# Optimization experiments

Measured on AMD Instinct MI355X. Metric: run time of the kernel, lower is better.

## Reference

```python
import jax, jax.numpy as jnp
import numpy as np

IM_H = 256.0
IM_W = 256.0


def setup_inputs() -> dict:
    key = jax.random.key(0)
    k1, k2 = jax.random.split(key)
    feats = jax.random.normal(k1, (8, 64, 64, 64), dtype=jnp.float32)
    Kcam = jax.random.normal(k2, (2, 4, 3, 4), dtype=jnp.float32)
    vmax = jnp.ones((2, 3), dtype=jnp.float32)
    vmin = jnp.zeros((2, 3), dtype=jnp.float32)
    return {"feats": feats, "Kcam": Kcam, "vmax": vmax, "vmin": vmin, "nvox": 48}


def reference(feats, Kcam, vmax, vmin, nvox):
    nR, fdim, fh, fw = feats.shape
    batch, view = Kcam.shape[0], Kcam.shape[1]
    rsz_h = float(fh) / IM_H
    rsz_w = float(fw) / IM_W

    # Build voxel grid per batch: linspace(vmin, vmax, nvox) along each axis.
    t = jnp.linspace(0.0, 1.0, nvox, dtype=jnp.float32)  # [nvox]
    rng = vmin[:, :, None] + (vmax - vmin)[:, :, None] * t  # [batch, 3, nvox]
    shp = (batch, nvox, nvox, nvox)
    gx = jnp.broadcast_to(rng[:, 0, :, None, None], shp)  # meshgrid 'ij' (torch default)
    gy = jnp.broadcast_to(rng[:, 1, None, :, None], shp)
    gz = jnp.broadcast_to(rng[:, 2, None, None, :], shp)
    grid = jnp.stack([gx, gy, gz], axis=1).reshape(batch, 3, -1)  # [batch, 3, nV]
    nV = grid.shape[2]
    rs_grid = jnp.concatenate([grid, jnp.ones((batch, 1, nV), jnp.float32)], axis=1)  # [batch, 4, nV]

    # Perspective projection: [batch, view*3, 4] @ [batch, 4, nV]
    im_p = jnp.einsum('bvrk,bkn->bvrn', Kcam, rs_grid).reshape(batch * view, 3, nV)
    im_x, im_y, im_z = im_p[:, 0, :], im_p[:, 1, :], im_p[:, 2, :]
    im_x = jnp.clip(im_x / im_z * rsz_w, 0.0, fw - 1)
    im_y = jnp.clip(im_y / im_z * rsz_h, 0.0, fh - 1)

    im_x0 = jnp.floor(im_x)
    im_x1 = jnp.clip(im_x0 + 1.0, 0.0, fw - 1)
    im_y0 = jnp.floor(im_y)
    im_y1 = jnp.clip(im_y0 + 1.0, 0.0, fh - 1)

    flat = feats.reshape(nR, fdim, fh * fw)  # [nR, fdim, fh*fw]

    def gather(xi, yi):
        idx = (yi * fw + xi).astype(jnp.int32)  # [nR, nV]
        return jax.vmap(lambda f, i: f[:, i])(flat, idx)  # [nR, fdim, nV]

    Ia = gather(im_x0, im_y0)
    Ib = gather(im_x0, im_y1)
    Ic = gather(im_x1, im_y0)
    Id = gather(im_x1, im_y1)

    wa = ((im_x1 - im_x) * (im_y1 - im_y))[:, None, :]
    wb = ((im_x1 - im_x) * (im_y - im_y0))[:, None, :]
    wc = ((im_x - im_x0) * (im_y1 - im_y))[:, None, :]
    wd = ((im_x - im_x0) * (im_y - im_y0))[:, None, :]

    Ibilin = wa * Ia + wb * Ib + wc * Ic + wd * Id  # [nR, fdim, nV]
    return Ibilin.reshape(nR, fdim, nvox, nvox, nvox)
```

## Files before the change

kernel.cpp:

```cpp
#include <hip/hip_runtime.h>


#define NR    8
#define FDIM  64
#define FH    64
#define FW    64
#define NVOX  48
#define NV    (NVOX * NVOX * NVOX)
#define VIEW  4

__global__ __launch_bounds__(256) void proj_splat_kernel(
    const float* __restrict__ feats,
    const float* __restrict__ Kcam,
    const float* __restrict__ vmax,
    const float* __restrict__ vmin,
    float* __restrict__ out)
{
    const int r = blockIdx.y;
    const int n = blockIdx.x * 256 + threadIdx.x;
    const int b = r >> 2;

    const int i   = n / (NVOX * NVOX);
    const int rem = n - i * (NVOX * NVOX);
    const int j   = rem / NVOX;
    const int k   = rem - j * NVOX;

    const float inv = 1.0f / (float)(NVOX - 1);
    const float tx = (float)i * inv;
    const float ty = (float)j * inv;
    const float tz = (float)k * inv;

    const float* vmn = vmin + b * 3;
    const float* vmx = vmax + b * 3;
    const float gx = vmn[0] + (vmx[0] - vmn[0]) * tx;
    const float gy = vmn[1] + (vmx[1] - vmn[1]) * ty;
    const float gz = vmn[2] + (vmx[2] - vmn[2]) * tz;

    const float* K = Kcam + r * 12;
    const float px = K[0] * gx + K[1] * gy + K[2]  * gz + K[3];
    const float py = K[4] * gx + K[5] * gy + K[6]  * gz + K[7];
    const float pz = K[8] * gx + K[9] * gy + K[10] * gz + K[11];

    const float rsz_w = (float)FW / 256.0f;
    const float rsz_h = (float)FH / 256.0f;

    float imx = px / pz * rsz_w;
    float imy = py / pz * rsz_h;
    imx = fminf(fmaxf(imx, 0.0f), (float)(FW - 1));
    imy = fminf(fmaxf(imy, 0.0f), (float)(FH - 1));

    const float x0 = floorf(imx);
    const float x1 = fminf(x0 + 1.0f, (float)(FW - 1));
    const float y0 = floorf(imy);
    const float y1 = fminf(y0 + 1.0f, (float)(FH - 1));

    const float wa = (x1 - imx) * (y1 - imy);
    const float wb = (x1 - imx) * (imy - y0);
    const float wc = (imx - x0) * (y1 - imy);
    const float wd = (imx - x0) * (imy - y0);

    const int ix0 = (int)x0, ix1 = (int)x1;
    const int iy0 = (int)y0, iy1 = (int)y1;
    const int i00 = iy0 * FW + ix0;
    const int i10 = iy1 * FW + ix0;
    const int i01 = iy0 * FW + ix1;
    const int i11 = iy1 * FW + ix1;

    const float* f = feats + (size_t)r * FDIM * FH * FW;
    float* o = out + (size_t)r * FDIM * NV + n;

#pragma unroll 4
    for (int c = 0; c < FDIM; ++c) {
        const float* fc = f + c * (FH * FW);
        const float Ia = fc[i00];
        const float Ib = fc[i10];
        const float Ic = fc[i01];
        const float Id = fc[i11];
        const float v = wa * Ia + wb * Ib + wc * Ic + wd * Id;
        __builtin_nontemporal_store(v, o + (size_t)c * NV);
    }
}

extern "C" void kernel_launch(void* const* d_in, const int* in_sizes, int n_in,
                              void* d_out, int out_size, void* d_ws, size_t ws_size,
                              hipStream_t stream) {
    const float* feats = (const float*)d_in[0];
    const float* Kcam  = (const float*)d_in[1];
    const float* vmax  = (const float*)d_in[2];
    const float* vmin  = (const float*)d_in[3];
    float* out = (float*)d_out;

    dim3 grid(NV / 256, NR);
    dim3 block(256);
    proj_splat_kernel<<<grid, block, 0, stream>>>(feats, Kcam, vmax, vmin, out);
}
```

Baseline: 274.9 us.

## Stage feature channels in LDS and compute four voxels per thread

Each block now takes a 16x8x16 voxel tile for one view. It streams the feature image through shared memory two channels at a time, prefetching the next pair into registers while the current pair is used. Each thread projects four consecutive z-voxels once, reads the bilinear taps from LDS instead of scattered global loads, and writes float4 nontemporal stores. This replaces per-voxel random global gathers with coalesced image loads and LDS lookups. In exchange, every tile re-reads the whole feature volume for its view, syncs twice per channel pair, and the grid shrinks to 432 blocks of 512 threads, which may leave some CUs idle.

```diff
diff --git a/kernel.cpp b/kernel.cpp
--- a/kernel.cpp
+++ b/kernel.cpp
@@ -5,79 +5,134 @@
 #define FDIM  64
 #define FH    64
 #define FW    64
+#define IMG   (FH * FW)
 #define NVOX  48
 #define NV    (NVOX * NVOX * NVOX)
-#define VIEW  4
+#define CPP   2
+#define NPH   (FDIM / CPP)
+#define TI    16
+#define TJ    8
+#define TK    16
+#define THREADS 512
 
-__global__ __launch_bounds__(256) void proj_splat_kernel(
+typedef float f32x4 __attribute__((ext_vector_type(4)));
+
+__global__ __launch_bounds__(THREADS, 4) void proj_splat_kernel(
     const float* __restrict__ feats,
     const float* __restrict__ Kcam,
     const float* __restrict__ vmax,
     const float* __restrict__ vmin,
     float* __restrict__ out)
 {
+    __shared__ float lds[CPP][IMG + 4];
+
+    const int t = threadIdx.x;
     const int r = blockIdx.y;
-    const int n = blockIdx.x * 256 + threadIdx.x;
     const int b = r >> 2;
 
-    const int i   = n / (NVOX * NVOX);
-    const int rem = n - i * (NVOX * NVOX);
-    const int j   = rem / NVOX;
-    const int k   = rem - j * NVOX;
+    const int tile = blockIdx.x;
+    const int ti = tile / 18;
+    const int tj = (tile / 3) % 6;
+    const int tk = tile % 3;
+
+    const int i_loc = t >> 5;
+    const int j_loc = (t >> 2) & 7;
+    const int k4    = t & 3;
+
+    const int vi  = ti * TI + i_loc;
+    const int vj  = tj * TJ + j_loc;
+    const int vk0 = tk * TK + k4 * 4;
 
     const float inv = 1.0f / (float)(NVOX - 1);
-    const float tx = (float)i * inv;
-    const float ty = (float)j * inv;
-    const float tz = (float)k * inv;
-
     const float* vmn = vmin + b * 3;
     const float* vmx = vmax + b * 3;
-    const float gx = vmn[0] + (vmx[0] - vmn[0]) * tx;
-    const float gy = vmn[1] + (vmx[1] - vmn[1]) * ty;
-    const float gz = vmn[2] + (vmx[2] - vmn[2]) * tz;
+    const float gx = vmn[0] + (vmx[0] - vmn[0]) * ((float)vi * inv);
+    const float gy = vmn[1] + (vmx[1] - vmn[1]) * ((float)vj * inv);
 
     const float* K = Kcam + r * 12;
-    const float px = K[0] * gx + K[1] * gy + K[2]  * gz + K[3];
-    const float py = K[4] * gx + K[5] * gy + K[6]  * gz + K[7];
-    const float pz = K[8] * gx + K[9] * gy + K[10] * gz + K[11];
+    const float pxc = K[0] * gx + K[1] * gy + K[3];
+    const float pyc = K[4] * gx + K[5] * gy + K[7];
+    const float pzc = K[8] * gx + K[9] * gy + K[11];
 
-    const float rsz_w = (float)FW / 256.0f;
-    const float rsz_h = (float)FH / 256.0f;
+    const float rsz = 0.25f;
 
-    float imx = px / pz * rsz_w;
-    float imy = py / pz * rsz_h;
-    imx = fminf(fmaxf(imx, 0.0f), (float)(FW - 1));
-    imy = fminf(fmaxf(imy, 0.0f), (float)(FH - 1));
+    int   idxA[4], idxB[4];
+    float wA0[4], wA1[4], wB0[4], wB1[4];
+#pragma unroll
+    for (int v = 0; v < 4; ++v) {
+        const float gz = vmn[2] + (vmx[2] - vmn[2]) * ((float)(vk0 + v) * inv);
+        const float px = pxc + K[2]  * gz;
+        const float py = pyc + K[6]  * gz;
+        const float pz = pzc + K[10] * gz;
 
-    const float x0 = floorf(imx);
-    const float x1 = fminf(x0 + 1.0f, (float)(FW - 1));
-    const float y0 = floorf(imy);
-    const float y1 = fminf(y0 + 1.0f, (float)(FH - 1));
+        float imx = px / pz * rsz;
+        float imy = py / pz * rsz;
+        imx = fminf(fmaxf(imx, 0.0f), (float)(FW - 1));
+        imy = fminf(fmaxf(imy, 0.0f), (float)(FH - 1));
 
-    const float wa = (x1 - imx) * (y1 - imy);
-    const float wb = (x1 - imx) * (imy - y0);
-    const float wc = (imx - x0) * (y1 - imy);
-    const float wd = (imx - x0) * (imy - y0);
+        const float x0 = floorf(imx);
+        const float x1 = fminf(x0 + 1.0f, (float)(FW - 1));
+        const float y0 = floorf(imy);
+        const float y1 = fminf(y0 + 1.0f, (float)(FH - 1));
 
-    const int ix0 = (int)x0, ix1 = (int)x1;
-    const int iy0 = (int)y0, iy1 = (int)y1;
-    const int i00 = iy0 * FW + ix0;
-    const int i10 = iy1 * FW + ix0;
-    const int i01 = iy0 * FW + ix1;
-    const int i11 = iy1 * FW + ix1;
+        wA0[v] = (x1 - imx) * (y1 - imy);
+        wA1[v] = (imx - x0) * (y1 - imy);
+        wB0[v] = (x1 - imx) * (imy - y0);
+        wB1[v] = (imx - x0) * (imy - y0);
 
-    const float* f = feats + (size_t)r * FDIM * FH * FW;
-    float* o = out + (size_t)r * FDIM * NV + n;
+        const int ix0 = (int)x0;
+        const int iy0 = (int)y0;
+        const int iy1 = (int)y1;
+        idxA[v] = iy0 * FW + ix0;
+        idxB[v] = iy1 * FW + ix0;
+    }
 
-#pragma unroll 4
-    for (int c = 0; c < FDIM; ++c) {
-        const float* fc = f + c * (FH * FW);
-        const float Ia = fc[i00];
-        const float Ib = fc[i10];
-        const float Ic = fc[i01];
-        const float Id = fc[i11];
-        const float v = wa * Ia + wb * Ib + wc * Ic + wd * Id;
-        __builtin_nontemporal_store(v, o + (size_t)c * NV);
+    if (t == 0) { lds[0][IMG] = 0.0f; lds[1][IMG] = 0.0f; }
+
+    const float* fbase = feats + (size_t)r * FDIM * IMG;
+    float* obase = out + (size_t)r * FDIM * NV + ((vi * NVOX + vj) * NVOX + vk0);
+
+    f32x4 sreg[2][CPP];
+#pragma unroll
+    for (int ci = 0; ci < CPP; ++ci)
+#pragma unroll
+        for (int q = 0; q < 2; ++q)
+            sreg[q][ci] = *reinterpret_cast<const f32x4*>(
+                fbase + (size_t)ci * IMG + q * 2048 + t * 4);
+
+    for (int p = 0; p < NPH; ++p) {
+#pragma unroll
+        for (int ci = 0; ci < CPP; ++ci)
+#pragma unroll
+            for (int q = 0; q < 2; ++q)
+                *reinterpret_cast<f32x4*>(&lds[ci][q * 2048 + t * 4]) = sreg[q][ci];
+        __syncthreads();
+
+        if (p + 1 < NPH) {
+#pragma unroll
+            for (int ci = 0; ci < CPP; ++ci)
+#pragma unroll
+                for (int q = 0; q < 2; ++q)
+                    sreg[q][ci] = *reinterpret_cast<const f32x4*>(
+                        fbase + (size_t)((p + 1) * CPP + ci) * IMG + q * 2048 + t * 4);
+        }
+
+#pragma unroll
+        for (int ci = 0; ci < CPP; ++ci) {
+            const int c = p * CPP + ci;
+            float acc[4];
+#pragma unroll
+            for (int v = 0; v < 4; ++v) {
+                const float A0 = lds[ci][idxA[v]];
+                const float A1 = lds[ci][idxA[v] + 1];
+                const float B0 = lds[ci][idxB[v]];
+                const float B1 = lds[ci][idxB[v] + 1];
+                acc[v] = wA0[v] * A0 + wA1[v] * A1 + wB0[v] * B0 + wB1[v] * B1;
+            }
+            f32x4 o4 = { acc[0], acc[1], acc[2], acc[3] };
+            __builtin_nontemporal_store(o4, reinterpret_cast<f32x4*>(obase + (size_t)c * NV));
+        }
+        __syncthreads();
     }
 }
 
@@ -90,7 +145,7 @@
     const float* vmin  = (const float*)d_in[3];
     float* out = (float*)d_out;
 
-    dim3 grid(NV / 256, NR);
-    dim3 block(256);
+    dim3 grid(54, NR);
+    dim3 block(THREADS);
     proj_splat_kernel<<<grid, block, 0, stream>>>(feats, Kcam, vmax, vmin, out);
 }
```

Measured after the change: 309.1 us. +12.4%, slower.

## Stage channel-pair feature planes in LDS and loop voxels per block

Applied to the files above, without the earlier changes.

Re-partitions work so each block owns two feature channels and a quarter of the voxels, loading both 64x64 planes into shared memory and doing bilinear gathers from LDS instead of global memory. Projection constants are folded into per-axis coefficients and voxel indices are advanced incrementally. The projection math is now recomputed per channel pair, and the x1 neighbor is read as ia+1, which relies on zero weights at the right edge.

```diff
diff --git a/kernel.cpp b/kernel.cpp
--- a/kernel.cpp
+++ b/kernel.cpp
@@ -5,79 +5,108 @@
 #define FDIM  64
 #define FH    64
 #define FW    64
+#define IMG   (FH * FW)
 #define NVOX  48
 #define NV    (NVOX * NVOX * NVOX)
-#define VIEW  4
+#define THREADS 256
+#define QUARTERS 4
+#define VPB   (NV / QUARTERS)
+#define ITERS (VPB / THREADS)
 
-__global__ __launch_bounds__(256) void proj_splat_kernel(
+typedef float f32x4 __attribute__((ext_vector_type(4)));
+
+__global__ __launch_bounds__(THREADS, 4) void proj_splat_kernel(
     const float* __restrict__ feats,
     const float* __restrict__ Kcam,
     const float* __restrict__ vmax,
     const float* __restrict__ vmin,
     float* __restrict__ out)
 {
-    const int r = blockIdx.y;
-    const int n = blockIdx.x * 256 + threadIdx.x;
-    const int b = r >> 2;
+    __shared__ float lds[2 * IMG + 1];
 
-    const int i   = n / (NVOX * NVOX);
-    const int rem = n - i * (NVOX * NVOX);
-    const int j   = rem / NVOX;
-    const int k   = rem - j * NVOX;
+    const int t  = threadIdx.x;
+    const int cp = blockIdx.x;
+    const int qq = blockIdx.y;
+    const int r  = blockIdx.z;
+    const int b  = r >> 2;
+
+    const float* src = feats + ((size_t)r * FDIM + 2 * cp) * IMG;
+#pragma unroll
+    for (int q = 0; q < 8; ++q) {
+        const int off = q * (THREADS * 4) + t * 4;
+        *reinterpret_cast<f32x4*>(&lds[off]) =
+            *reinterpret_cast<const f32x4*>(src + off);
+    }
+    if (t == 0) lds[2 * IMG] = 0.0f;
+    __syncthreads();
 
     const float inv = 1.0f / (float)(NVOX - 1);
-    const float tx = (float)i * inv;
-    const float ty = (float)j * inv;
-    const float tz = (float)k * inv;
-
     const float* vmn = vmin + b * 3;
     const float* vmx = vmax + b * 3;
-    const float gx = vmn[0] + (vmx[0] - vmn[0]) * tx;
-    const float gy = vmn[1] + (vmx[1] - vmn[1]) * ty;
-    const float gz = vmn[2] + (vmx[2] - vmn[2]) * tz;
+    const float ax = (vmx[0] - vmn[0]) * inv;
+    const float ay = (vmx[1] - vmn[1]) * inv;
+    const float az = (vmx[2] - vmn[2]) * inv;
+    const float* K = Kcam + r * 12;
+    const float A0 = K[0] * ax, B0 = K[1] * ay, D0 = K[2]  * az;
+    const float C0 = K[0] * vmn[0] + K[1] * vmn[1] + K[2]  * vmn[2] + K[3];
+    const float A1 = K[4] * ax, B1 = K[5] * ay, D1 = K[6]  * az;
+    const float C1 = K[4] * vmn[0] + K[5] * vmn[1] + K[6]  * vmn[2] + K[7];
+    const float A2 = K[8] * ax, B2 = K[9] * ay, D2 = K[10] * az;
+    const float C2 = K[8] * vmn[0] + K[9] * vmn[1] + K[10] * vmn[2] + K[11];
 
-    const float* K = Kcam + r * 12;
-    const float px = K[0] * gx + K[1] * gy + K[2]  * gz + K[3];
-    const float py = K[4] * gx + K[5] * gy + K[6]  * gz + K[7];
-    const float pz = K[8] * gx + K[9] * gy + K[10] * gz + K[11];
+    float* o0 = out + ((size_t)r * FDIM + 2 * cp) * NV;
+    float* o1 = o0 + NV;
 
-    const float rsz_w = (float)FW / 256.0f;
-    const float rsz_h = (float)FH / 256.0f;
+    int n = qq * VPB + t;
+    int i = n / (NVOX * NVOX);
+    int j = (n / NVOX) % NVOX;
+    int k = n % NVOX;
 
-    float imx = px / pz * rsz_w;
-    float imy = py / pz * rsz_h;
-    imx = fminf(fmaxf(imx, 0.0f), (float)(FW - 1));
-    imy = fminf(fmaxf(imy, 0.0f), (float)(FH - 1));
+    for (int it = 0; it < ITERS; ++it) {
+        const float fi = (float)i, fj = (float)j, fk = (float)k;
+        const float px = C0 + A0 * fi + B0 * fj + D0 * fk;
+        const float py = C1 + A1 * fi + B1 * fj + D1 * fk;
+        const float pz = C2 + A2 * fi + B2 * fj + D2 * fk;
 
-    const float x0 = floorf(imx);
-    const float x1 = fminf(x0 + 1.0f, (float)(FW - 1));
-    const float y0 = floorf(imy);
-    const float y1 = fminf(y0 + 1.0f, (float)(FH - 1));
+        const float rz = 0.25f / pz;
+        float imx = px * rz;
+        float imy = py * rz;
+        imx = fminf(fmaxf(imx, 0.0f), (float)(FW - 1));
+        imy = fminf(fmaxf(imy, 0.0f), (float)(FH - 1));
 
-    const float wa = (x1 - imx) * (y1 - imy);
-    const float wb = (x1 - imx) * (imy - y0);
-    const float wc = (imx - x0) * (y1 - imy);
-    const float wd = (imx - x0) * (imy - y0);
+        const float x0 = floorf(imx);
+        const float x1 = fminf(x0 + 1.0f, (float)(FW - 1));
+        const float y0 = floorf(imy);
+        const float y1 = fminf(y0 + 1.0f, (float)(FH - 1));
 
-    const int ix0 = (int)x0, ix1 = (int)x1;
-    const int iy0 = (int)y0, iy1 = (int)y1;
-    const int i00 = iy0 * FW + ix0;
-    const int i10 = iy1 * FW + ix0;
-    const int i01 = iy0 * FW + ix1;
-    const int i11 = iy1 * FW + ix1;
+        const float wa = (x1 - imx) * (y1 - imy);
+        const float wc = (imx - x0) * (y1 - imy);
+        const float wb = (x1 - imx) * (imy - y0);
+        const float wd = (imx - x0) * (imy - y0);
 
-    const float* f = feats + (size_t)r * FDIM * FH * FW;
-    float* o = out + (size_t)r * FDIM * NV + n;
+        const int ix0 = (int)x0;
+        const int iy0 = (int)y0;
+        const int iy1 = (int)y1;
+        const int ia = iy0 * FW + ix0;
+        const int ib = iy1 * FW + ix0;
 
-#pragma unroll 4
-    for (int c = 0; c < FDIM; ++c) {
-        const float* fc = f + c * (FH * FW);
-        const float Ia = fc[i00];
-        const float Ib = fc[i10];
-        const float Ic = fc[i01];
-        const float Id = fc[i11];
-        const float v = wa * Ia + wb * Ib + wc * Ic + wd * Id;
-        __builtin_nontemporal_store(v, o + (size_t)c * NV);
+        {
+            const float a0 = lds[ia],       a1 = lds[ia + 1];
+            const float b0 = lds[ib],       b1 = lds[ib + 1];
+            const float res = wa * a0 + wc * a1 + wb * b0 + wd * b1;
+            __builtin_nontemporal_store(res, o0 + n);
+        }
+        {
+            const float a0 = lds[IMG + ia], a1 = lds[IMG + ia + 1];
+            const float b0 = lds[IMG + ib], b1 = lds[IMG + ib + 1];
+            const float res = wa * a0 + wc * a1 + wb * b0 + wd * b1;
+            __builtin_nontemporal_store(res, o1 + n);
+        }
+
+        n += THREADS;
+        k += 16;
+        if (k >= NVOX) { k -= NVOX; j += 6; } else { j += 5; }
+        if (j >= NVOX) { j -= NVOX; i += 1; }
     }
 }
 
@@ -90,7 +119,7 @@
     const float* vmin  = (const float*)d_in[3];
     float* out = (float*)d_out;
 
-    dim3 grid(NV / 256, NR);
-    dim3 block(256);
+    dim3 grid(FDIM / 2, QUARTERS, NR);
+    dim3 block(THREADS);
     proj_splat_kernel<<<grid, block, 0, stream>>>(feats, Kcam, vmax, vmin, out);
 }
```

Result: faster. 242.9 us (-11.6%).
